# Optimization experiments

Measured on AMD Instinct MI355X. Metric: run time of the kernel, lower is better.

The kernel has to match this reference:

```python
import jax, jax.numpy as jnp
import numpy as np

N_NODES = 50000
N_EDGES = 800000
IN_CH = 128
HIDDEN = [128, 128]
OUT_CH = 64


def _glorot(key, shape):
    fan_in, fan_out = shape
    lim = (6.0 / (fan_in + fan_out)) ** 0.5
    return jax.random.uniform(key, shape, jnp.float32, -lim, lim)


def setup_inputs() -> dict:
    key = jax.random.key(0)
    ks = jax.random.split(key, 12)
    x = jax.random.normal(ks[0], (N_NODES, IN_CH), jnp.float32)
    edge_index = jax.random.randint(ks[1], (2, N_EDGES), 0, N_NODES, jnp.int64)
    dims = [IN_CH] + HIDDEN + [OUT_CH]
    params = {}
    for i in range(len(dims) - 1):
        d_in, d_out = dims[i], dims[i + 1]
        params[f"W_l{i}"] = _glorot(ks[2 + 3 * i], (d_in, d_out))      # neighbor weight
        params[f"W_r{i}"] = _glorot(ks[3 + 3 * i], (d_in, d_out))      # root/self weight
        params[f"b{i}"] = jnp.zeros((d_out,), jnp.float32)
    return {"x": x, "edge_index": edge_index, **params}


def _sage_conv(x, src, dst, W_l, W_r, b):
    # mean-aggregate neighbor features: messages flow src -> dst
    n = x.shape[0]
    agg = jax.ops.segment_sum(x[src], dst, num_segments=n)            # [N, d_in]
    cnt = jax.ops.segment_sum(jnp.ones((src.shape[0],), x.dtype), dst, num_segments=n)
    mean = agg / jnp.maximum(cnt, 1.0)[:, None]
    # PyG SAGEConv: lin_l(mean_neighbors) + lin_r(x_self); bias on lin_l only
    return mean @ W_l + x @ W_r + b


def reference(x, edge_index,
              W_l0, W_r0, b0,
              W_l1, W_r1, b1,
              W_l2, W_r2, b2):
    src, dst = edge_index[0], edge_index[1]
    h = _sage_conv(x, src, dst, W_l0, W_r0, b0)
    h = jax.nn.elu(h)
    h = _sage_conv(h, src, dst, W_l1, W_r1, b1)
    h = jax.nn.elu(h)
    out = _sage_conv(h, src, dst, W_l2, W_r2, b2)
    return out
```

## Files before the change

### kernel.cpp

```cpp
#include <hip/hip_runtime.h>
#include <math.h>

#define N_NODES 50000
#define N_EDGES 800000
#define IN_CH 128
#define NBUCK 196
#define BCAP 5120
#define EPB 4082

typedef unsigned short ushort_t;
typedef unsigned int uint_t;
typedef __attribute__((ext_vector_type(8))) short bf16x8;
typedef __attribute__((ext_vector_type(4))) float f32x4;

static __device__ __forceinline__ ushort_t f32_to_bf16(float f) {
    uint_t u = __float_as_uint(f);
    uint_t r = (u + 0x7fffu + ((u >> 16) & 1u)) >> 16;
    return (ushort_t)r;
}

__global__ __launch_bounds__(256) void binA(
    const int* __restrict__ src, const int* __restrict__ dst,
    uint_t* __restrict__ gbcnt, uint_t* __restrict__ gbuck) {
    __shared__ uint_t hist[NBUCK];
    __shared__ uint_t excl_s[NBUCK];
    __shared__ uint_t gbase[NBUCK];
    __shared__ uint_t cur[NBUCK];
    __shared__ uint_t pfx[256];
    __shared__ uint_t stage[4096];
    __shared__ uint_t gpos[4096];
    const int t = threadIdx.x;
    const int e0 = blockIdx.x * EPB;
    const int e1 = min(e0 + EPB, N_EDGES);

    for (int i = t; i < NBUCK; i += 256) hist[i] = 0;
    __syncthreads();
    for (int e = e0 + t; e < e1; e += 256) atomicAdd(&hist[dst[e] >> 8], 1u);
    __syncthreads();
    uint_t own = (t < NBUCK) ? hist[t] : 0;
    pfx[t] = own;
    __syncthreads();
    for (int d = 1; d < 256; d <<= 1) {
        uint_t v = (t >= d) ? pfx[t - d] : 0;
        __syncthreads();
        pfx[t] += v;
        __syncthreads();
    }
    if (t < NBUCK) {
        uint_t excl = pfx[t] - own;
        excl_s[t] = excl;
        cur[t] = excl;
        gbase[t] = atomicAdd(&gbcnt[t], own);
    }
    __syncthreads();
    for (int e = e0 + t; e < e1; e += 256) {
        int d_ = dst[e];
        int b = d_ >> 8;
        uint_t p = atomicAdd(&cur[b], 1u);
        stage[p] = ((uint_t)(d_ & 255) << 16) | (uint_t)src[e];
        gpos[p] = (uint_t)b * BCAP + gbase[b] + (p - excl_s[b]);
    }
    __syncthreads();
    const int n = e1 - e0;
    for (int i = t; i < n; i += 256) gbuck[gpos[i]] = stage[i];
}

__global__ __launch_bounds__(256) void binB1(
    const uint_t* __restrict__ gbcnt, const uint_t* __restrict__ gbuck,
    int* __restrict__ degi) {
    __shared__ uint_t h[256];
    const int b = blockIdx.x;
    const int t = threadIdx.x;
    h[t] = 0;
    __syncthreads();
    const uint_t n = gbcnt[b];
    const uint_t* p = &gbuck[(size_t)b * BCAP];
    for (uint_t i = t; i < n; i += 256) atomicAdd(&h[(p[i] >> 16) & 255u], 1u);
    __syncthreads();
    int node = b * 256 + t;
    if (node < N_NODES) degi[node] = (int)h[t];
}

__global__ __launch_bounds__(256) void scan_p1(const int* __restrict__ degi,
                                               int* __restrict__ bsum, int n) {
    __shared__ int s[256];
    const int t = threadIdx.x;
    const int i = blockIdx.x * 256 + t;
    s[t] = (i < n) ? degi[i] : 0;
    __syncthreads();
    for (int d = 128; d > 0; d >>= 1) {
        if (t < d) s[t] += s[t + d];
        __syncthreads();
    }
    if (t == 0) bsum[blockIdx.x] = s[0];
}

__global__ __launch_bounds__(256) void scan_p2(int* __restrict__ bsum, int nb) {
    __shared__ int s[256];
    const int t = threadIdx.x;
    int v = (t < nb) ? bsum[t] : 0;
    s[t] = v;
    __syncthreads();
    for (int d = 1; d < 256; d <<= 1) {
        int u = (t >= d) ? s[t - d] : 0;
        __syncthreads();
        s[t] += u;
        __syncthreads();
    }
    if (t < nb) bsum[t] = s[t] - v;
}

__global__ __launch_bounds__(256) void scan_p3(const int* __restrict__ degi,
                                               const int* __restrict__ bsum,
                                               int* __restrict__ offs, int n) {
    __shared__ int s[256];
    const int t = threadIdx.x;
    const int i = blockIdx.x * 256 + t;
    int v = (i < n) ? degi[i] : 0;
    s[t] = v;
    __syncthreads();
    for (int d = 1; d < 256; d <<= 1) {
        int u = (t >= d) ? s[t - d] : 0;
        __syncthreads();
        s[t] += u;
        __syncthreads();
    }
    if (i < n) offs[i] = s[t] - v + bsum[blockIdx.x];
    if (i == 0) offs[n] = N_EDGES;
}

__global__ __launch_bounds__(256) void binB2(
    const uint_t* __restrict__ gbcnt, const uint_t* __restrict__ gbuck,
    const int* __restrict__ offs, int* __restrict__ ebuf) {
    __shared__ int cur[256];
    __shared__ int stage[BCAP];
    const int b = blockIdx.x;
    const int t = threadIdx.x;
    const int node = b * 256 + t;
    const int obase = offs[b * 256];
    cur[t] = (node < N_NODES) ? (offs[node] - obase) : 0;
    __syncthreads();
    const uint_t n = gbcnt[b];
    const uint_t* p = &gbuck[(size_t)b * BCAP];
    for (uint_t i = t; i < n; i += 256) {
        uint_t pr_ = p[i];
        int l = (pr_ >> 16) & 255;
        int pos = atomicAdd(&cur[l], 1);
        stage[pos] = (int)(pr_ & 0xFFFFu);
    }
    __syncthreads();
    for (uint_t i = t; i < n; i += 256) ebuf[obase + (int)i] = stage[i];
}

__global__ __launch_bounds__(256) void cvt_x(const float* __restrict__ x,
                                             ushort_t* __restrict__ xb, int n8) {
    int i = blockIdx.x * 256 + threadIdx.x;
    if (i >= n8) return;
    const float* p = x + (size_t)i * 8;
    float4 lo = *(const float4*)p;
    float4 hi = *(const float4*)(p + 4);
    bf16x8 r;
    r[0] = (short)f32_to_bf16(lo.x); r[1] = (short)f32_to_bf16(lo.y);
    r[2] = (short)f32_to_bf16(lo.z); r[3] = (short)f32_to_bf16(lo.w);
    r[4] = (short)f32_to_bf16(hi.x); r[5] = (short)f32_to_bf16(hi.y);
    r[6] = (short)f32_to_bf16(hi.z); r[7] = (short)f32_to_bf16(hi.w);
    *(bf16x8*)&xb[(size_t)i * 8] = r;
}

template <int C>
__global__ __launch_bounds__(256) void prep_w(const float* __restrict__ Wl,
                                              const float* __restrict__ Wr,
                                              ushort_t* __restrict__ Bt) {
    int i = blockIdx.x * 256 + threadIdx.x;
    if (i >= C * 256) return;
    int c = i / 256, k = i % 256;
    float v = (k < 128) ? Wl[(size_t)k * C + c] : Wr[(size_t)(k - 128) * C + c];
    Bt[i] = f32_to_bf16(v);
}

__global__ __launch_bounds__(256) void gather_mean(
    const int* __restrict__ offs, const int* __restrict__ ebuf,
    const ushort_t* __restrict__ feat, ushort_t* __restrict__ M, int nNodes) {
    const int wid = (int)((blockIdx.x * 256u + threadIdx.x) >> 6);
    const int lane = threadIdx.x & 63;
    if (wid >= nNodes) return;
    const int o0 = offs[wid], o1 = offs[wid + 1];
    const float inv = 1.0f / fmaxf((float)(o1 - o0), 1.0f);
    const int c = lane * 2;

    float ax0 = 0, ay0 = 0, ax1 = 0, ay1 = 0, ax2 = 0, ay2 = 0, ax3 = 0, ay3 = 0;
    int j = o0;
    for (; j + 4 <= o1; j += 4) {
        int s0 = ebuf[j], s1 = ebuf[j + 1], s2 = ebuf[j + 2], s3 = ebuf[j + 3];
        uint_t v0 = *(const uint_t*)&feat[(size_t)s0 * 128 + c];
        uint_t v1 = *(const uint_t*)&feat[(size_t)s1 * 128 + c];
        uint_t v2 = *(const uint_t*)&feat[(size_t)s2 * 128 + c];
        uint_t v3 = *(const uint_t*)&feat[(size_t)s3 * 128 + c];
        ax0 += __uint_as_float(v0 << 16); ay0 += __uint_as_float(v0 & 0xffff0000u);
        ax1 += __uint_as_float(v1 << 16); ay1 += __uint_as_float(v1 & 0xffff0000u);
        ax2 += __uint_as_float(v2 << 16); ay2 += __uint_as_float(v2 & 0xffff0000u);
        ax3 += __uint_as_float(v3 << 16); ay3 += __uint_as_float(v3 & 0xffff0000u);
    }
    for (; j < o1; ++j) {
        uint_t v0 = *(const uint_t*)&feat[(size_t)ebuf[j] * 128 + c];
        ax0 += __uint_as_float(v0 << 16);
        ay0 += __uint_as_float(v0 & 0xffff0000u);
    }
    float vx = (ax0 + ax1 + ax2 + ax3) * inv;
    float vy = (ay0 + ay1 + ay2 + ay3) * inv;
    uint_t packed = (uint_t)f32_to_bf16(vx) | ((uint_t)f32_to_bf16(vy) << 16);
    *(uint_t*)&M[(size_t)wid * 128 + c] = packed;
}

template <int C, bool ELU, bool OUT_F32>
__global__ __launch_bounds__(256) void gemm_fused(
    const ushort_t* __restrict__ M, const ushort_t* __restrict__ X,
    const ushort_t* __restrict__ Bt, const float* __restrict__ bias,
    void* __restrict__ out_v, int nNodes) {
    const int tid = threadIdx.x;
    const int wave = tid >> 6, lane = tid & 63;
    const int lrow = lane & 15, lgrp = lane >> 4;
    const int rowbase = blockIdx.x * 64 + (wave >> 1) * 32;
    const int colbase = blockIdx.y * 64 + (wave & 1) * 32;

    f32x4 acc[2][2] = {};

#pragma unroll
    for (int half = 0; half < 2; ++half) {
        const ushort_t* A = half ? X : M;
#pragma unroll
        for (int ks = 0; ks < 4; ++ks) {
            const int k0 = ks * 32 + lgrp * 8;
            bf16x8 a[2], bf[2];
#pragma unroll
            for (int mi = 0; mi < 2; ++mi) {
                int r = rowbase + mi * 16 + lrow;
                r = min(r, nNodes - 1);
                a[mi] = *(const bf16x8*)&A[(size_t)r * 128 + k0];
            }
#pragma unroll
            for (int ni = 0; ni < 2; ++ni) {
                int c = colbase + ni * 16 + lrow;
                bf[ni] = *(const bf16x8*)&Bt[(size_t)c * 256 + half * 128 + k0];
            }
#pragma unroll
            for (int mi = 0; mi < 2; ++mi)
#pragma unroll
                for (int ni = 0; ni < 2; ++ni)
                    acc[mi][ni] = __builtin_amdgcn_mfma_f32_16x16x32_bf16(
                        a[mi], bf[ni], acc[mi][ni], 0, 0, 0);
        }
    }

#pragma unroll
    for (int ni = 0; ni < 2; ++ni) {
        const int c = colbase + ni * 16 + lrow;
        const float bv = bias[c];
#pragma unroll
        for (int mi = 0; mi < 2; ++mi) {
#pragma unroll
            for (int j = 0; j < 4; ++j) {
                int r = rowbase + mi * 16 + lgrp * 4 + j;
                if (r >= nNodes) continue;
                float v = acc[mi][ni][j] + bv;
                if (ELU) v = v > 0.f ? v : expm1f(v);
                if (OUT_F32) ((float*)out_v)[(size_t)r * C + c] = v;
                else ((ushort_t*)out_v)[(size_t)r * C + c] = f32_to_bf16(v);
            }
        }
    }
}

extern "C" void kernel_launch(void* const* d_in, const int* in_sizes, int n_in,
                              void* d_out, int out_size, void* d_ws, size_t ws_size,
                              hipStream_t stream) {
    const float* x = (const float*)d_in[0];
    const int* ei = (const int*)d_in[1];
    const int* src = ei;
    const int* dst = ei + N_EDGES;
    const float* Wl0 = (const float*)d_in[2];
    const float* Wr0 = (const float*)d_in[3];
    const float* b0 = (const float*)d_in[4];
    const float* Wl1 = (const float*)d_in[5];
    const float* Wr1 = (const float*)d_in[6];
    const float* b1 = (const float*)d_in[7];
    const float* Wl2 = (const float*)d_in[8];
    const float* Wr2 = (const float*)d_in[9];
    const float* b2 = (const float*)d_in[10];
    float* out = (float*)d_out;

    int* wsi = (int*)d_ws;
    int* degi = wsi;
    int* offs = degi + 51200;
    int* bsum = offs + 51200;
    uint_t* gbcnt = (uint_t*)(bsum + 256);
    int* ebuf = (int*)(gbcnt + 256);
    uint_t* gbuck = (uint_t*)(ebuf + 800000);
    ushort_t* Bt0 = (ushort_t*)(gbuck + NBUCK * BCAP);
    ushort_t* Bt1 = Bt0 + 128 * 256;
    ushort_t* Bt2 = Bt1 + 128 * 256;
    const long long NB = (long long)N_NODES * 128;
    ushort_t* xb = Bt2 + 64 * 256;
    ushort_t* Mb = xb + NB;
    ushort_t* hA = Mb + NB;
    ushort_t* hB = hA + NB;

    const int NSB = (N_NODES + 255) / 256;

    hipMemsetAsync(gbcnt, 0, NBUCK * sizeof(uint_t), stream);
    binA<<<NBUCK, 256, 0, stream>>>(src, dst, gbcnt, gbuck);
    binB1<<<NBUCK, 256, 0, stream>>>(gbcnt, gbuck, degi);
    scan_p1<<<NSB, 256, 0, stream>>>(degi, bsum, N_NODES);
    scan_p2<<<1, 256, 0, stream>>>(bsum, NSB);
    scan_p3<<<NSB, 256, 0, stream>>>(degi, bsum, offs, N_NODES);
    binB2<<<NBUCK, 256, 0, stream>>>(gbcnt, gbuck, offs, ebuf);

    cvt_x<<<(N_NODES * 16 + 255) / 256, 256, 0, stream>>>(x, xb, N_NODES * 16);
    prep_w<128><<<(128 * 256 + 255) / 256, 256, 0, stream>>>(Wl0, Wr0, Bt0);
    prep_w<128><<<(128 * 256 + 255) / 256, 256, 0, stream>>>(Wl1, Wr1, Bt1);
    prep_w<64><<<(64 * 256 + 255) / 256, 256, 0, stream>>>(Wl2, Wr2, Bt2);

    const int GATHER_GRID = (N_NODES * 64 + 255) / 256;
    const int GR = (N_NODES + 63) / 64;

    gather_mean<<<GATHER_GRID, 256, 0, stream>>>(offs, ebuf, xb, Mb, N_NODES);
    gemm_fused<128, true, false><<<dim3(GR, 2), 256, 0, stream>>>(
        Mb, xb, Bt0, b0, hA, N_NODES);

    gather_mean<<<GATHER_GRID, 256, 0, stream>>>(offs, ebuf, hA, Mb, N_NODES);
    gemm_fused<128, true, false><<<dim3(GR, 2), 256, 0, stream>>>(
        Mb, hA, Bt1, b1, hB, N_NODES);

    gather_mean<<<GATHER_GRID, 256, 0, stream>>>(offs, ebuf, hB, Mb, N_NODES);
    gemm_fused<64, false, true><<<dim3(GR, 1), 256, 0, stream>>>(
        Mb, hB, Bt2, b2, out, N_NODES);
}
```

Baseline: 248.3 us.

## Fuse CSR build kernels, merge weight prep, widen gather loads

```diff
diff --git a/kernel.cpp b/kernel.cpp
--- a/kernel.cpp
+++ b/kernel.cpp
@@ -65,96 +65,64 @@
     for (int i = t; i < n; i += 256) gbuck[gpos[i]] = stage[i];
 }
 
-__global__ __launch_bounds__(256) void binB1(
+__global__ __launch_bounds__(256) void binB(
     const uint_t* __restrict__ gbcnt, const uint_t* __restrict__ gbuck,
-    int* __restrict__ degi) {
+    int* __restrict__ offs, int* __restrict__ ebuf) {
+    __shared__ uint_t pairs[BCAP];
+    __shared__ int stage[BCAP];
+    __shared__ uint_t bscan[256];
     __shared__ uint_t h[256];
+    __shared__ uint_t psc[256];
+    __shared__ int cur[256];
     const int b = blockIdx.x;
     const int t = threadIdx.x;
+
+    uint_t g = (t < NBUCK) ? gbcnt[t] : 0;
+    bscan[t] = g;
+    __syncthreads();
+    for (int d = 1; d < 256; d <<= 1) {
+        uint_t v = (t >= d) ? bscan[t - d] : 0;
+        __syncthreads();
+        bscan[t] += v;
+        __syncthreads();
+    }
+    const int base = (b > 0) ? (int)bscan[b - 1] : 0;
+    const uint_t n = gbcnt[b];
+
+    for (uint_t i = t; i < n; i += 256) pairs[i] = gbuck[(size_t)b * BCAP + i];
     h[t] = 0;
     __syncthreads();
-    const uint_t n = gbcnt[b];
-    const uint_t* p = &gbuck[(size_t)b * BCAP];
-    for (uint_t i = t; i < n; i += 256) atomicAdd(&h[(p[i] >> 16) & 255u], 1u);
-    __syncthreads();
-    int node = b * 256 + t;
-    if (node < N_NODES) degi[node] = (int)h[t];
-}
-
-__global__ __launch_bounds__(256) void scan_p1(const int* __restrict__ degi,
-                                               int* __restrict__ bsum, int n) {
-    __shared__ int s[256];
-    const int t = threadIdx.x;
-    const int i = blockIdx.x * 256 + t;
-    s[t] = (i < n) ? degi[i] : 0;
-    __syncthreads();
-    for (int d = 128; d > 0; d >>= 1) {
-        if (t < d) s[t] += s[t + d];
-        __syncthreads();
-    }
-    if (t == 0) bsum[blockIdx.x] = s[0];
-}
-
-__global__ __launch_bounds__(256) void scan_p2(int* __restrict__ bsum, int nb) {
-    __shared__ int s[256];
-    const int t = threadIdx.x;
-    int v = (t < nb) ? bsum[t] : 0;
-    s[t] = v;
+    for (uint_t i = t; i < n; i += 256) atomicAdd(&h[(pairs[i] >> 16) & 255u], 1u);
+    __syncthreads();
+    uint_t own = h[t];
+    psc[t] = own;
     __syncthreads();
     for (int d = 1; d < 256; d <<= 1) {
-        int u = (t >= d) ? s[t - d] : 0;
-        __syncthreads();
-        s[t] += u;
-        __syncthreads();
-    }
-    if (t < nb) bsum[t] = s[t] - v;
-}
-
-__global__ __launch_bounds__(256) void scan_p3(const int* __restrict__ degi,
-                                               const int* __restrict__ bsum,
-                                               int* __restrict__ offs, int n) {
-    __shared__ int s[256];
-    const int t = threadIdx.x;
-    const int i = blockIdx.x * 256 + t;
-    int v = (i < n) ? degi[i] : 0;
-    s[t] = v;
-    __syncthreads();
-    for (int d = 1; d < 256; d <<= 1) {
-        int u = (t >= d) ? s[t - d] : 0;
-        __syncthreads();
-        s[t] += u;
-        __syncthreads();
-    }
-    if (i < n) offs[i] = s[t] - v + bsum[blockIdx.x];
-    if (i == 0) offs[n] = N_EDGES;
-}
-
-__global__ __launch_bounds__(256) void binB2(
-    const uint_t* __restrict__ gbcnt, const uint_t* __restrict__ gbuck,
-    const int* __restrict__ offs, int* __restrict__ ebuf) {
-    __shared__ int cur[256];
-    __shared__ int stage[BCAP];
-    const int b = blockIdx.x;
-    const int t = threadIdx.x;
+        uint_t v = (t >= d) ? psc[t - d] : 0;
+        __syncthreads();
+        psc[t] += v;
+        __syncthreads();
+    }
+    const int excl = (int)(psc[t] - own);
     const int node = b * 256 + t;
-    const int obase = offs[b * 256];
-    cur[t] = (node < N_NODES) ? (offs[node] - obase) : 0;
-    __syncthreads();
-    const uint_t n = gbcnt[b];
-    const uint_t* p = &gbuck[(size_t)b * BCAP];
+    if (node <= N_NODES) offs[node] = base + excl;
+    cur[t] = excl;
+    __syncthreads();
     for (uint_t i = t; i < n; i += 256) {
-        uint_t pr_ = p[i];
-        int l = (pr_ >> 16) & 255;
+        uint_t p = pairs[i];
+        int l = (p >> 16) & 255;
         int pos = atomicAdd(&cur[l], 1);
-        stage[pos] = (int)(pr_ & 0xFFFFu);
-    }
-    __syncthreads();
-    for (uint_t i = t; i < n; i += 256) ebuf[obase + (int)i] = stage[i];
+        stage[pos] = (int)(p & 0xFFFFu);
+    }
+    __syncthreads();
+    for (uint_t i = t; i < n; i += 256) ebuf[base + (int)i] = stage[i];
 }
 
 __global__ __launch_bounds__(256) void cvt_x(const float* __restrict__ x,
-                                             ushort_t* __restrict__ xb, int n8) {
+                                             ushort_t* __restrict__ xb,
+                                             uint_t* __restrict__ gbcnt, int n8) {
     int i = blockIdx.x * 256 + threadIdx.x;
+    if (blockIdx.x == 0 && threadIdx.x < NBUCK) gbcnt[threadIdx.x] = 0;
     if (i >= n8) return;
     const float* p = x + (size_t)i * 8;
     float4 lo = *(const float4*)p;
@@ -167,12 +135,26 @@
     *(bf16x8*)&xb[(size_t)i * 8] = r;
 }
 
-template <int C>
-__global__ __launch_bounds__(256) void prep_w(const float* __restrict__ Wl,
-                                              const float* __restrict__ Wr,
-                                              ushort_t* __restrict__ Bt) {
+__global__ __launch_bounds__(256) void prep_all(
+    const float* __restrict__ Wl0, const float* __restrict__ Wr0,
+    const float* __restrict__ Wl1, const float* __restrict__ Wr1,
+    const float* __restrict__ Wl2, const float* __restrict__ Wr2,
+    ushort_t* __restrict__ Bt0, ushort_t* __restrict__ Bt1,
+    ushort_t* __restrict__ Bt2) {
     int i = blockIdx.x * 256 + threadIdx.x;
-    if (i >= C * 256) return;
+    const float* Wl;
+    const float* Wr;
+    ushort_t* Bt;
+    int C;
+    if (i < 32768) {
+        Wl = Wl0; Wr = Wr0; Bt = Bt0; C = 128;
+    } else if (i < 65536) {
+        i -= 32768; Wl = Wl1; Wr = Wr1; Bt = Bt1; C = 128;
+    } else if (i < 81920) {
+        i -= 65536; Wl = Wl2; Wr = Wr2; Bt = Bt2; C = 64;
+    } else {
+        return;
+    }
     int c = i / 256, k = i % 256;
     float v = (k < 128) ? Wl[(size_t)k * C + c] : Wr[(size_t)(k - 128) * C + c];
     Bt[i] = f32_to_bf16(v);
@@ -186,30 +168,45 @@
     if (wid >= nNodes) return;
     const int o0 = offs[wid], o1 = offs[wid + 1];
     const float inv = 1.0f / fmaxf((float)(o1 - o0), 1.0f);
-    const int c = lane * 2;
-
-    float ax0 = 0, ay0 = 0, ax1 = 0, ay1 = 0, ax2 = 0, ay2 = 0, ax3 = 0, ay3 = 0;
+    const int half = lane >> 5;
+    const int cl = (lane & 31) * 4;
+
+    float a00 = 0, a01 = 0, a02 = 0, a03 = 0;
+    float a10 = 0, a11 = 0, a12 = 0, a13 = 0;
     int j = o0;
     for (; j + 4 <= o1; j += 4) {
-        int s0 = ebuf[j], s1 = ebuf[j + 1], s2 = ebuf[j + 2], s3 = ebuf[j + 3];
-        uint_t v0 = *(const uint_t*)&feat[(size_t)s0 * 128 + c];
-        uint_t v1 = *(const uint_t*)&feat[(size_t)s1 * 128 + c];
-        uint_t v2 = *(const uint_t*)&feat[(size_t)s2 * 128 + c];
-        uint_t v3 = *(const uint_t*)&feat[(size_t)s3 * 128 + c];
-        ax0 += __uint_as_float(v0 << 16); ay0 += __uint_as_float(v0 & 0xffff0000u);
-        ax1 += __uint_as_float(v1 << 16); ay1 += __uint_as_float(v1 & 0xffff0000u);
-        ax2 += __uint_as_float(v2 << 16); ay2 += __uint_as_float(v2 & 0xffff0000u);
-        ax3 += __uint_as_float(v3 << 16); ay3 += __uint_as_float(v3 & 0xffff0000u);
-    }
-    for (; j < o1; ++j) {
-        uint_t v0 = *(const uint_t*)&feat[(size_t)ebuf[j] * 128 + c];
-        ax0 += __uint_as_float(v0 << 16);
-        ay0 += __uint_as_float(v0 & 0xffff0000u);
-    }
-    float vx = (ax0 + ax1 + ax2 + ax3) * inv;
-    float vy = (ay0 + ay1 + ay2 + ay3) * inv;
-    uint_t packed = (uint_t)f32_to_bf16(vx) | ((uint_t)f32_to_bf16(vy) << 16);
-    *(uint_t*)&M[(size_t)wid * 128 + c] = packed;
+        int s0 = ebuf[j + half];
+        int s1 = ebuf[j + 2 + half];
+        uint2 v0 = *(const uint2*)&feat[(size_t)s0 * 128 + cl];
+        uint2 v1 = *(const uint2*)&feat[(size_t)s1 * 128 + cl];
+        a00 += __uint_as_float(v0.x << 16); a01 += __uint_as_float(v0.x & 0xffff0000u);
+        a02 += __uint_as_float(v0.y << 16); a03 += __uint_as_float(v0.y & 0xffff0000u);
+        a10 += __uint_as_float(v1.x << 16); a11 += __uint_as_float(v1.x & 0xffff0000u);
+        a12 += __uint_as_float(v1.y << 16); a13 += __uint_as_float(v1.y & 0xffff0000u);
+    }
+    for (; j + 2 <= o1; j += 2) {
+        int s0 = ebuf[j + half];
+        uint2 v0 = *(const uint2*)&feat[(size_t)s0 * 128 + cl];
+        a00 += __uint_as_float(v0.x << 16); a01 += __uint_as_float(v0.x & 0xffff0000u);
+        a02 += __uint_as_float(v0.y << 16); a03 += __uint_as_float(v0.y & 0xffff0000u);
+    }
+    if (j < o1 && half == 0) {
+        int s0 = ebuf[j];
+        uint2 v0 = *(const uint2*)&feat[(size_t)s0 * 128 + cl];
+        a00 += __uint_as_float(v0.x << 16); a01 += __uint_as_float(v0.x & 0xffff0000u);
+        a02 += __uint_as_float(v0.y << 16); a03 += __uint_as_float(v0.y & 0xffff0000u);
+    }
+    float t0 = a00 + a10, t1 = a01 + a11, t2 = a02 + a12, t3 = a03 + a13;
+    t0 += __shfl_xor(t0, 32);
+    t1 += __shfl_xor(t1, 32);
+    t2 += __shfl_xor(t2, 32);
+    t3 += __shfl_xor(t3, 32);
+    if (half == 0) {
+        uint2 o;
+        o.x = (uint_t)f32_to_bf16(t0 * inv) | ((uint_t)f32_to_bf16(t1 * inv) << 16);
+        o.y = (uint_t)f32_to_bf16(t2 * inv) | ((uint_t)f32_to_bf16(t3 * inv) << 16);
+        *(uint2*)&M[(size_t)wid * 128 + cl] = o;
+    }
 }
 
 template <int C, bool ELU, bool OUT_F32>
@@ -290,10 +287,8 @@
     float* out = (float*)d_out;
 
     int* wsi = (int*)d_ws;
-    int* degi = wsi;
-    int* offs = degi + 51200;
-    int* bsum = offs + 51200;
-    uint_t* gbcnt = (uint_t*)(bsum + 256);
+    int* offs = wsi;
+    uint_t* gbcnt = (uint_t*)(offs + 51200);
     int* ebuf = (int*)(gbcnt + 256);
     uint_t* gbuck = (uint_t*)(ebuf + 800000);
     ushort_t* Bt0 = (ushort_t*)(gbuck + NBUCK * BCAP);
@@ -305,20 +300,12 @@
     ushort_t* hA = Mb + NB;
     ushort_t* hB = hA + NB;
 
-    const int NSB = (N_NODES + 255) / 256;
-
-    hipMemsetAsync(gbcnt, 0, NBUCK * sizeof(uint_t), stream);
+    cvt_x<<<(N_NODES * 16 + 255) / 256, 256, 0, stream>>>(x, xb, gbcnt, N_NODES * 16);
+    prep_all<<<(81920 + 255) / 256, 256, 0, stream>>>(
+        Wl0, Wr0, Wl1, Wr1, Wl2, Wr2, Bt0, Bt1, Bt2);
+
     binA<<<NBUCK, 256, 0, stream>>>(src, dst, gbcnt, gbuck);
-    binB1<<<NBUCK, 256, 0, stream>>>(gbcnt, gbuck, degi);
-    scan_p1<<<NSB, 256, 0, stream>>>(degi, bsum, N_NODES);
-    scan_p2<<<1, 256, 0, stream>>>(bsum, NSB);
-    scan_p3<<<NSB, 256, 0, stream>>>(degi, bsum, offs, N_NODES);
-    binB2<<<NBUCK, 256, 0, stream>>>(gbcnt, gbuck, offs, ebuf);
-
-    cvt_x<<<(N_NODES * 16 + 255) / 256, 256, 0, stream>>>(x, xb, N_NODES * 16);
-    prep_w<128><<<(128 * 256 + 255) / 256, 256, 0, stream>>>(Wl0, Wr0, Bt0);
-    prep_w<128><<<(128 * 256 + 255) / 256, 256, 0, stream>>>(Wl1, Wr1, Bt1);
-    prep_w<64><<<(64 * 256 + 255) / 256, 256, 0, stream>>>(Wl2, Wr2, Bt2);
+    binB<<<NBUCK, 256, 0, stream>>>(gbcnt, gbuck, offs, ebuf);
 
     const int GATHER_GRID = (N_NODES * 64 + 255) / 256;
     const int GR = (N_NODES + 63) / 64;
```

Result: no change. 249.3 us (+0.4%).
